# Performance work log

Measured on AMD Instinct MI355X. Metric: run time of the kernel, lower is better.

## Reference

```python
import jax, jax.numpy as jnp
import numpy as np
from jax import lax

L, S, H, D_IN, D_OUT = 4, 64, 256, 768, 768
B, T = 8, 2048
EPS = 1e-5


def _xavier(key, shape):
    fan_out, fan_in = shape[-2], shape[-1]
    limit = (6.0 / (fan_in + fan_out)) ** 0.5
    return jax.random.uniform(key, shape, jnp.float32, -limit, limit)


def setup_inputs() -> dict:
    key = jax.random.key(0)
    ks = jax.random.split(key, 12)
    return {
        "x": jax.random.normal(ks[0], (B, T, D_IN), jnp.float32),
        "in_proj_w": _xavier(ks[1], (H, D_IN)),
        "in_proj_b": jnp.zeros((H,), jnp.float32),
        "ln_g": jnp.ones((L, H), jnp.float32),
        "ln_b": jnp.zeros((L, H), jnp.float32),
        "ip_w": _xavier(ks[2], (L, S, H)),
        "ip_b": jnp.zeros((L, S), jnp.float32),
        "A": jax.random.normal(ks[3], (L, S, S), jnp.float32) * 0.1,
        "Bv": jax.random.normal(ks[4], (L, S), jnp.float32) * 0.1,
        "Cm": jax.random.normal(ks[5], (L, H, S), jnp.float32) * 0.1,
        "bias_A": jnp.zeros((L, S), jnp.float32),
        "bias_C": jnp.zeros((L, H), jnp.float32),
        "gate_w": _xavier(ks[6], (L, H, H)),
        "gate_b": jnp.zeros((L, H), jnp.float32),
        "proj_w": _xavier(ks[7], (L, H, H)),
        "proj_b": jnp.zeros((L, H), jnp.float32),
        "out_proj_w": _xavier(ks[8], (D_OUT, H)),
        "out_proj_b": jnp.zeros((D_OUT,), jnp.float32),
    }


def _layer_norm(x, g, b):
    mu = jnp.mean(x, axis=-1, keepdims=True)
    var = jnp.mean(jnp.square(x - mu), axis=-1, keepdims=True)
    return (x - mu) * lax.rsqrt(var + EPS) * g + b


def _ssm_layer(xn, ip_w, ip_b, A, Bv, Cm, bias_A, bias_C, gate_w, gate_b, proj_w, proj_b):
    # xn: [B, T, H]
    x_state = jnp.einsum("bth,sh->bts", xn, ip_w) + ip_b          # [B,T,S]
    gate = jax.nn.sigmoid(jnp.einsum("bth,gh->btg", xn, gate_w) + gate_b)  # [B,T,H]

    def step(h, xs_t):
        # h: [B,S], xs_t: [B,S]
        h = jnp.clip(h @ A.T + Bv * xs_t + bias_A, -10.0, 10.0)
        y = h @ Cm.T + bias_C                                     # [B,H]
        return h, y

    h0 = jnp.zeros((xn.shape[0], A.shape[0]), xn.dtype)
    _, ys = lax.scan(step, h0, jnp.swapaxes(x_state, 0, 1))        # ys: [T,B,H]
    y = jnp.swapaxes(ys, 0, 1)                                     # [B,T,H]
    y = jnp.einsum("bth,oh->bto", y, proj_w) + proj_b
    return gate * y + (1.0 - gate) * xn


def reference(x, in_proj_w, in_proj_b, ln_g, ln_b, ip_w, ip_b, A, Bv, Cm,
              bias_A, bias_C, gate_w, gate_b, proj_w, proj_b, out_proj_w, out_proj_b):
    h = jnp.einsum("btd,hd->bth", x, in_proj_w) + in_proj_b
    for i in range(L):
        xn = _layer_norm(h, ln_g[i], ln_b[i])
        h = h + _ssm_layer(xn, ip_w[i], ip_b[i], A[i], Bv[i], Cm[i],
                           bias_A[i], bias_C[i], gate_w[i], gate_b[i],
                           proj_w[i], proj_b[i])
    return jnp.einsum("bth,oh->bto", h, out_proj_w) + out_proj_b
```

## Files before the change

### kernel.cpp

```cpp
#include <hip/hip_runtime.h>

typedef float f32x4 __attribute__((ext_vector_type(4)));
typedef short short8 __attribute__((ext_vector_type(8)));

#define T_LEN 2048
#define HD 256
#define SD 64
#define DIN 768
#define DOUT 768
#define NCHUNK 32
#define CLEN 64

#define SBAR() __builtin_amdgcn_sched_barrier(0)

__device__ __forceinline__ unsigned short f2bf(float f) {
    unsigned int u = __float_as_uint(f);
    unsigned int r = u + 0x7FFFu + ((u >> 16) & 1u);
    return (unsigned short)(r >> 16);
}
__device__ __forceinline__ float bf2f(unsigned short h) {
    return __uint_as_float(((unsigned int)h) << 16);
}
__device__ __forceinline__ int swz(int row, int col, int stride) {
    return row * stride + (col ^ ((row & 7) << 3));
}
#define GLL(gp, lp) __builtin_amdgcn_global_load_lds( \
    (const __attribute__((address_space(1))) void*)(gp), \
    (__attribute__((address_space(3))) void*)(lp), 16, 0, 0)

__global__ __launch_bounds__(256) void cvt_w_k(const float* __restrict__ s0, const float* __restrict__ s1,
                                               const float* __restrict__ s2, const float* __restrict__ s3,
                                               const float* __restrict__ s4, const float* __restrict__ s5,
                                               unsigned short* __restrict__ d) {
    int i = blockIdx.x * 256 + threadIdx.x;
    if (i >= 1048576) return;
    float v;
    if (i < 196608)      v = s0[i];
    else if (i < 262144) v = s1[i - 196608];
    else if (i < 524288) v = s2[i - 262144];
    else if (i < 786432) v = s3[i - 524288];
    else if (i < 851968) v = s4[i - 786432];
    else                 v = s5[i - 851968];
    d[i] = f2bf(v);
}

__global__ __launch_bounds__(256) void matpow_k(const float* __restrict__ A, float* __restrict__ Apow) {
    __shared__ unsigned short Mh[4096], Ml[4096], MhT[4096], MlT[4096];
    const int l = blockIdx.x, tid = threadIdx.x;
    const int w = tid >> 6, ln = tid & 63, ll = ln & 15, lh = ln >> 4;
    const float* src = A + l * 4096;
    for (int i = tid; i < 4096; i += 256) {
        float v = src[i];
        unsigned short hi = f2bf(v);
        unsigned short lo = f2bf(v - bf2f(hi));
        int r = i >> 6, c = i & 63;
        Mh[swz(r, c, 64)] = hi;  Ml[swz(r, c, 64)] = lo;
        MhT[swz(c, r, 64)] = hi; MlT[swz(c, r, 64)] = lo;
    }
    __syncthreads();
    for (int it = 0; it < 6; it++) {
        f32x4 acc[4] = {};
#pragma unroll
        for (int ks = 0; ks < 2; ks++) {
            int ar = w * 16 + ll, c0 = ks * 32 + lh * 8;
            short8 ah = *reinterpret_cast<const short8*>(&Mh[swz(ar, c0, 64)]);
            short8 al = *reinterpret_cast<const short8*>(&Ml[swz(ar, c0, 64)]);
#pragma unroll
            for (int nf = 0; nf < 4; nf++) {
                int br = nf * 16 + ll;
                short8 bh = *reinterpret_cast<const short8*>(&MhT[swz(br, c0, 64)]);
                short8 bl = *reinterpret_cast<const short8*>(&MlT[swz(br, c0, 64)]);
                acc[nf] = __builtin_amdgcn_mfma_f32_16x16x32_bf16(ah, bh, acc[nf], 0, 0, 0);
                acc[nf] = __builtin_amdgcn_mfma_f32_16x16x32_bf16(ah, bl, acc[nf], 0, 0, 0);
                acc[nf] = __builtin_amdgcn_mfma_f32_16x16x32_bf16(al, bh, acc[nf], 0, 0, 0);
            }
        }
        __syncthreads();
#pragma unroll
        for (int nf = 0; nf < 4; nf++)
#pragma unroll
            for (int r = 0; r < 4; r++) {
                float v = acc[nf][r];
                int row = w * 16 + lh * 4 + r, col = nf * 16 + ll;
                unsigned short hi = f2bf(v);
                unsigned short lo = f2bf(v - bf2f(hi));
                Mh[swz(row, col, 64)] = hi;  Ml[swz(row, col, 64)] = lo;
                MhT[swz(col, row, 64)] = hi; MlT[swz(col, row, 64)] = lo;
            }
        __syncthreads();
    }
    for (int i = tid; i < 4096; i += 256) {
        int r = i >> 6, c = i & 63;
        Apow[l * 4096 + i] = bf2f(Mh[swz(r, c, 64)]) + bf2f(Ml[swz(r, c, 64)]);
    }
}

__global__ __launch_bounds__(256) void in_ln_k(const float* __restrict__ x,
                                               const unsigned short* __restrict__ w_in,
                                               const float* __restrict__ inb,
                                               const float* __restrict__ lng, const float* __restrict__ lnb,
                                               unsigned short* __restrict__ hb, unsigned short* __restrict__ xnb) {
    __shared__ unsigned short smem[8192 + 32 * 264];
    unsigned short* Ws = smem;
    unsigned short* hnb = smem + 8192;
    const int tid = threadIdx.x, l = tid & 63, w = tid >> 6;
    const int ll = l & 15, lh = l >> 4;
    const int mf = w >> 1, nh = w & 1;
    const int m0 = blockIdx.x * 32;
    const float* ap = x + (size_t)(m0 + mf * 16 + ll) * DIN + lh * 8;
    const unsigned short* gwb = w_in + (size_t)(w * 64 + (l >> 2)) * DIN + (l & 3) * 8;
    unsigned short* lwb = &Ws[(w * 64) * 32];
    f32x4 acc[8] = {};
    for (int k0 = 0; k0 < DIN; k0 += 32) {
#pragma unroll
        for (int q = 0; q < 4; q++)
            GLL(gwb + (size_t)(q * 16) * DIN + k0, lwb + q * 16 * 32);
        float4 a0 = *reinterpret_cast<const float4*>(ap + k0);
        float4 a1 = *reinterpret_cast<const float4*>(ap + k0 + 4);
        short8 af;
        af[0] = (short)f2bf(a0.x); af[1] = (short)f2bf(a0.y);
        af[2] = (short)f2bf(a0.z); af[3] = (short)f2bf(a0.w);
        af[4] = (short)f2bf(a1.x); af[5] = (short)f2bf(a1.y);
        af[6] = (short)f2bf(a1.z); af[7] = (short)f2bf(a1.w);
        __syncthreads();
#pragma unroll
        for (int j = 0; j < 8; j++) {
            short8 b = *reinterpret_cast<const short8*>(&Ws[(size_t)(nh * 128 + j * 16 + ll) * 32 + lh * 8]);
            acc[j] = __builtin_amdgcn_mfma_f32_16x16x32_bf16(af, b, acc[j], 0, 0, 0);
        }
        __syncthreads();
    }
#pragma unroll
    for (int j = 0; j < 8; j++)
#pragma unroll
        for (int r = 0; r < 4; r++) {
            int rowl = mf * 16 + lh * 4 + r;
            int col = nh * 128 + j * 16 + ll;
            hnb[rowl * 264 + col] = f2bf(acc[j][r] + inb[col]);
        }
    __syncthreads();
#pragma unroll
    for (int q = 0; q < 8; q++) {
        int rowl = w * 8 + q;
        size_t gidx = (size_t)(m0 + rowl) * HD + l * 4;
        ushort4 hv = *reinterpret_cast<const ushort4*>(&hnb[rowl * 264 + l * 4]);
        float o0 = bf2f(hv.x), o1 = bf2f(hv.y), o2 = bf2f(hv.z), o3 = bf2f(hv.w);
        float s = o0 + o1 + o2 + o3;
        float s2 = o0 * o0 + o1 * o1 + o2 * o2 + o3 * o3;
#pragma unroll
        for (int mm = 1; mm < 64; mm <<= 1) { s += __shfl_xor(s, mm); s2 += __shfl_xor(s2, mm); }
        float mean = s * (1.f / 256.f);
        float var = s2 * (1.f / 256.f) - mean * mean;
        float rstd = rsqrtf(var + 1e-5f);
        int c = l * 4;
        *reinterpret_cast<ushort4*>(hb + gidx) = hv;
        ushort4 xo;
        xo.x = f2bf((o0 - mean) * rstd * lng[c + 0] + lnb[c + 0]);
        xo.y = f2bf((o1 - mean) * rstd * lng[c + 1] + lnb[c + 1]);
        xo.z = f2bf((o2 - mean) * rstd * lng[c + 2] + lnb[c + 2]);
        xo.w = f2bf((o3 - mean) * rstd * lng[c + 3] + lnb[c + 3]);
        *reinterpret_cast<ushort4*>(xnb + gidx) = xo;
    }
}

__device__ __forceinline__ void staged_core256(const unsigned short* __restrict__ A, int m0b,
                                               const unsigned short* __restrict__ W, int n0,
                                               unsigned short* As, unsigned short* Bs,
                                               int tid, f32x4 (*acc)[4]) {
    const int l = tid & 63, w = tid >> 6;
    const int ll = l & 15, lh = l >> 4;
    const int lr = l >> 2, lc = (l & 3) * 8;
    const unsigned short* ga1 = A + (size_t)(m0b + w * 32 + lr) * 256 + lc;
    const unsigned short* ga2 = ga1 + 16 * 256;
    const unsigned short* gb  = W + (size_t)(n0 + w * 16 + lr) * 256 + lc;
    unsigned short* la1 = As + w * 1024;
    unsigned short* la2 = As + w * 1024 + 512;
    unsigned short* lb  = Bs + w * 512;
#pragma unroll
    for (int k0 = 0; k0 < 256; k0 += 32) {
        GLL(ga1 + k0, la1);
        GLL(ga2 + k0, la2);
        GLL(gb + k0, lb);
        __syncthreads();
        short8 a0 = *reinterpret_cast<const short8*>(&As[(w * 32 + ll) * 32 + lh * 8]);
        short8 a1 = *reinterpret_cast<const short8*>(&As[(w * 32 + 16 + ll) * 32 + lh * 8]);
        short8 b0 = *reinterpret_cast<const short8*>(&Bs[(ll) * 32 + lh * 8]);
        short8 b1 = *reinterpret_cast<const short8*>(&Bs[(16 + ll) * 32 + lh * 8]);
        short8 b2 = *reinterpret_cast<const short8*>(&Bs[(32 + ll) * 32 + lh * 8]);
        short8 b3 = *reinterpret_cast<const short8*>(&Bs[(48 + ll) * 32 + lh * 8]);
        acc[0][0] = __builtin_amdgcn_mfma_f32_16x16x32_bf16(a0, b0, acc[0][0], 0, 0, 0);
        acc[0][1] = __builtin_amdgcn_mfma_f32_16x16x32_bf16(a0, b1, acc[0][1], 0, 0, 0);
        acc[0][2] = __builtin_amdgcn_mfma_f32_16x16x32_bf16(a0, b2, acc[0][2], 0, 0, 0);
        acc[0][3] = __builtin_amdgcn_mfma_f32_16x16x32_bf16(a0, b3, acc[0][3], 0, 0, 0);
        acc[1][0] = __builtin_amdgcn_mfma_f32_16x16x32_bf16(a1, b0, acc[1][0], 0, 0, 0);
        acc[1][1] = __builtin_amdgcn_mfma_f32_16x16x32_bf16(a1, b1, acc[1][1], 0, 0, 0);
        acc[1][2] = __builtin_amdgcn_mfma_f32_16x16x32_bf16(a1, b2, acc[1][2], 0, 0, 0);
        acc[1][3] = __builtin_amdgcn_mfma_f32_16x16x32_bf16(a1, b3, acc[1][3], 0, 0, 0);
        __syncthreads();
    }
}

template <int N>
__global__ __launch_bounds__(256) void gemm_k(const unsigned short* __restrict__ A,
                                              const unsigned short* __restrict__ W,
                                              const float* __restrict__ bias,
                                              float* __restrict__ outf) {
    __shared__ char smem[128 * 68 * 4];
    unsigned short* As = (unsigned short*)smem;
    unsigned short* Bs = As + 4096;
    float* sf = (float*)smem;
    const int tid = threadIdx.x, l = tid & 63, w = tid >> 6;
    const int ll = l & 15, lh = l >> 4;
    const int m0b = blockIdx.x * 128;
    const int n0 = blockIdx.y * 64;
    f32x4 acc[2][4] = {};
    staged_core256(A, m0b, W, n0, As, Bs, tid, acc);
#pragma unroll
    for (int mf = 0; mf < 2; mf++)
#pragma unroll
        for (int nf = 0; nf < 4; nf++)
#pragma unroll
            for (int r = 0; r < 4; r++) {
                int rowl = w * 32 + mf * 16 + lh * 4 + r;
                int col = nf * 16 + ll;
                sf[rowl * 68 + col] = acc[mf][nf][r] + bias[n0 + col];
            }
    __syncthreads();
#pragma unroll
    for (int p = 0; p < 8; p++) {
        int rowl = p * 16 + (tid >> 4);
        int col = (tid & 15) * 4;
        f32x4 v = *reinterpret_cast<const f32x4*>(&sf[rowl * 68 + col]);
        __builtin_nontemporal_store(v, reinterpret_cast<f32x4*>(outf + (size_t)(m0b + rowl) * N + n0 + col));
    }
}

__global__ __launch_bounds__(256) void gateip_k(const unsigned short* __restrict__ xnb,
                                                const unsigned short* __restrict__ wg,
                                                const unsigned short* __restrict__ wip,
                                                const float* __restrict__ gbias, const float* __restrict__ ipb,
                                                const float* __restrict__ Bv, const float* __restrict__ bA,
                                                unsigned short* __restrict__ gB, float* __restrict__ u) {
    __shared__ char smem[128 * 68 * 4];
    unsigned short* As = (unsigned short*)smem;
    unsigned short* Bs = As + 4096;
    float* sf = (float*)smem;
    unsigned short* su = (unsigned short*)smem;
    const int tid = threadIdx.x, l = tid & 63, w = tid >> 6;
    const int ll = l & 15, lh = l >> 4;
    const int m0b = blockIdx.x * 128;
    const int y = blockIdx.y;
    const bool gate = (y < 4);
    const int n0 = gate ? y * 64 : 0;
    f32x4 acc[2][4] = {};
    staged_core256(xnb, m0b, gate ? wg : wip, n0, As, Bs, tid, acc);
    if (gate) {
#pragma unroll
        for (int mf = 0; mf < 2; mf++)
#pragma unroll
            for (int nf = 0; nf < 4; nf++)
#pragma unroll
                for (int r = 0; r < 4; r++) {
                    int rowl = w * 32 + mf * 16 + lh * 4 + r;
                    int col = nf * 16 + ll;
                    float v = acc[mf][nf][r] + gbias[n0 + col];
                    su[rowl * 72 + col] = f2bf(1.f / (1.f + __expf(-v)));
                }
        __syncthreads();
#pragma unroll
        for (int p = 0; p < 8; p++) {
            int rowl = p * 16 + (tid >> 4);
            int col = (tid & 15) * 4;
            ushort4 v = *reinterpret_cast<const ushort4*>(&su[rowl * 72 + col]);
            *reinterpret_cast<ushort4*>(gB + (size_t)(m0b + rowl) * HD + n0 + col) = v;
        }
    } else {
#pragma unroll
        for (int mf = 0; mf < 2; mf++)
#pragma unroll
            for (int nf = 0; nf < 4; nf++)
#pragma unroll
                for (int r = 0; r < 4; r++) {
                    int rowl = w * 32 + mf * 16 + lh * 4 + r;
                    int col = nf * 16 + ll;
                    float v = acc[mf][nf][r] + ipb[col];
                    sf[rowl * 68 + col] = Bv[col] * v + bA[col];
                }
        __syncthreads();
#pragma unroll
        for (int p = 0; p < 8; p++) {
            int rowl = p * 16 + (tid >> 4);
            int col = (tid & 15) * 4;
            int m = m0b + rowl;
            int t = m & 2047, b2 = m >> 11;
            float4 v = *reinterpret_cast<const float4*>(&sf[rowl * 68 + col]);
            *reinterpret_cast<float4*>(u + ((size_t)((t << 3) + b2)) * 64 + col) = v;
        }
    }
}

template <bool LAST>
__global__ __launch_bounds__(256) void post3_k(const unsigned short* __restrict__ Hs,
                                               const unsigned short* __restrict__ wc,
                                               const float* __restrict__ bC,
                                               const unsigned short* __restrict__ wp,
                                               const float* __restrict__ pb,
                                               const unsigned short* __restrict__ gB,
                                               unsigned short* __restrict__ xnb,
                                               unsigned short* __restrict__ hb,
                                               const float* __restrict__ lng2, const float* __restrict__ lnb2) {
    __shared__ unsigned short ys[32 * 256];
    __shared__ unsigned short hnb[32 * 264];
    const int tid = threadIdx.x, l = tid & 63, w = tid >> 6;
    const int ll = l & 15, lh = l >> 4;
    const int mf = w >> 1, nh = w & 1;
    const int m0 = blockIdx.x * 32;
    {
        short8 ha[2], cb[8][2];
        const unsigned short* Ap = Hs + (size_t)(m0 + mf * 16 + ll) * SD + lh * 8;
#pragma unroll
        for (int ks = 0; ks < 2; ks++)
            ha[ks] = *reinterpret_cast<const short8*>(Ap + ks * 32);
#pragma unroll
        for (int ks = 0; ks < 2; ks++)
#pragma unroll
            for (int j = 0; j < 8; j++)
                cb[j][ks] = *reinterpret_cast<const short8*>(wc + (size_t)((nh * 8 + j) * 16 + ll) * SD + ks * 32 + lh * 8);
        SBAR();
        f32x4 acc[8] = {};
#pragma unroll
        for (int ks = 0; ks < 2; ks++)
#pragma unroll
            for (int j = 0; j < 8; j++)
                acc[j] = __builtin_amdgcn_mfma_f32_16x16x32_bf16(ha[ks], cb[j][ks], acc[j], 0, 0, 0);
#pragma unroll
        for (int j = 0; j < 8; j++)
#pragma unroll
            for (int r = 0; r < 4; r++) {
                int rowl = mf * 16 + lh * 4 + r;
                int col = (nh * 8 + j) * 16 + ll;
                ys[swz(rowl, col, 256)] = f2bf(acc[j][r] + bC[col]);
            }
    }
    __syncthreads();
    {
        f32x4 acc2[8] = {};
        const int arow = mf * 16 + ll;
#pragma unroll
        for (int kb = 0; kb < 4; kb++) {
            short8 pwf[8][2];
#pragma unroll
            for (int ks = 0; ks < 2; ks++)
#pragma unroll
                for (int j = 0; j < 8; j++)
                    pwf[j][ks] = *reinterpret_cast<const short8*>(wp + (size_t)((nh * 8 + j) * 16 + ll) * HD + kb * 64 + ks * 32 + lh * 8);
            SBAR();
#pragma unroll
            for (int ks = 0; ks < 2; ks++) {
                int c0 = kb * 64 + ks * 32 + lh * 8;
                short8 a = *reinterpret_cast<const short8*>(&ys[swz(arow, c0, 256)]);
#pragma unroll
                for (int j = 0; j < 8; j++)
                    acc2[j] = __builtin_amdgcn_mfma_f32_16x16x32_bf16(a, pwf[j][ks], acc2[j], 0, 0, 0);
            }
        }
#pragma unroll
        for (int j = 0; j < 8; j++)
#pragma unroll
            for (int r = 0; r < 4; r++) {
                int rowl = mf * 16 + lh * 4 + r;
                int col = (nh * 8 + j) * 16 + ll;
                hnb[rowl * 264 + col] = f2bf(acc2[j][r] + pb[col]);
            }
    }
    __syncthreads();
#pragma unroll
    for (int q = 0; q < 8; q++) {
        int rowl = w * 8 + q;
        int m = m0 + rowl;
        int t = m >> 3, b2 = m & 7;
        size_t gidx = ((size_t)((b2 << 11) + t)) * HD + l * 4;
        ushort4 hv = *reinterpret_cast<const ushort4*>(hb + gidx);
        ushort4 gv = *reinterpret_cast<const ushort4*>(gB + gidx);
        ushort4 xv = *reinterpret_cast<const ushort4*>(xnb + gidx);
        ushort4 yv = *reinterpret_cast<const ushort4*>(&hnb[rowl * 264 + l * 4]);
        float g0 = bf2f(gv.x), g1 = bf2f(gv.y), g2 = bf2f(gv.z), g3 = bf2f(gv.w);
        float o0 = bf2f(hv.x) + g0 * bf2f(yv.x) + (1.f - g0) * bf2f(xv.x);
        float o1 = bf2f(hv.y) + g1 * bf2f(yv.y) + (1.f - g1) * bf2f(xv.y);
        float o2 = bf2f(hv.z) + g2 * bf2f(yv.z) + (1.f - g2) * bf2f(xv.z);
        float o3 = bf2f(hv.w) + g3 * bf2f(yv.w) + (1.f - g3) * bf2f(xv.w);
        ushort4 hbv;
        hbv.x = f2bf(o0); hbv.y = f2bf(o1); hbv.z = f2bf(o2); hbv.w = f2bf(o3);
        *reinterpret_cast<ushort4*>(hb + gidx) = hbv;
        if constexpr (!LAST) {
            float s = o0 + o1 + o2 + o3;
            float s2 = o0 * o0 + o1 * o1 + o2 * o2 + o3 * o3;
#pragma unroll
            for (int mm = 1; mm < 64; mm <<= 1) { s += __shfl_xor(s, mm); s2 += __shfl_xor(s2, mm); }
            float mean = s * (1.f / 256.f);
            float var = s2 * (1.f / 256.f) - mean * mean;
            float rstd = rsqrtf(var + 1e-5f);
            int c = l * 4;
            ushort4 xo;
            xo.x = f2bf((o0 - mean) * rstd * lng2[c + 0] + lnb2[c + 0]);
            xo.y = f2bf((o1 - mean) * rstd * lng2[c + 1] + lnb2[c + 1]);
            xo.z = f2bf((o2 - mean) * rstd * lng2[c + 2] + lnb2[c + 2]);
            xo.w = f2bf((o3 - mean) * rstd * lng2[c + 3] + lnb2[c + 3]);
            *reinterpret_cast<ushort4*>(xnb + gidx) = xo;
        }
    }
}

__device__ __forceinline__ void loadA64(const float* __restrict__ Af, int s, float* a) {
#pragma unroll
    for (int q = 0; q < 16; q++) {
        float4 v = reinterpret_cast<const float4*>(Af + s * 64)[q];
        a[q * 4 + 0] = v.x; a[q * 4 + 1] = v.y; a[q * 4 + 2] = v.z; a[q * 4 + 3] = v.w;
    }
}

__device__ __forceinline__ float step64(const float* a, float h, float uu) {
    float ac0 = uu, ac1 = 0.f, ac2 = 0.f, ac3 = 0.f;
#pragma unroll
    for (int k = 0; k < 64; k += 4) {
        float b0 = __int_as_float(__builtin_amdgcn_readlane(__float_as_int(h), k + 0));
        float b1 = __int_as_float(__builtin_amdgcn_readlane(__float_as_int(h), k + 1));
        float b2 = __int_as_float(__builtin_amdgcn_readlane(__float_as_int(h), k + 2));
        float b3 = __int_as_float(__builtin_amdgcn_readlane(__float_as_int(h), k + 3));
        ac0 = fmaf(b0, a[k + 0], ac0);
        ac1 = fmaf(b1, a[k + 1], ac1);
        ac2 = fmaf(b2, a[k + 2], ac2);
        ac3 = fmaf(b3, a[k + 3], ac3);
    }
    return (ac0 + ac1) + (ac2 + ac3);
}

__global__ __launch_bounds__(64) void scan_chunk_k(const float* __restrict__ Af,
                                                   const float* __restrict__ u,
                                                   float* __restrict__ Slast) {
    const int c = blockIdx.x >> 3, b = blockIdx.x & 7;
    const int s = threadIdx.x;
    float a[64];
    loadA64(Af, s, a);
    const float* up = u + (c * CLEN) * 512 + b * 64 + s;
    float uv[CLEN];
#pragma unroll
    for (int i = 0; i < CLEN; i++) uv[i] = up[i * 512];
    float h = 0.f;
#pragma unroll
    for (int i = 0; i < CLEN; i++) h = step64(a, h, uv[i]);
    Slast[blockIdx.x * 64 + s] = h;
}

__global__ __launch_bounds__(64) void replay_k(const float* __restrict__ Af,
                                               const float* __restrict__ Apow,
                                               const float* __restrict__ u,
                                               const float* __restrict__ Slast,
                                               unsigned short* __restrict__ Hs,
                                               int* __restrict__ flag) {
    const int c = blockIdx.x >> 3, b = blockIdx.x & 7;
    const int s = threadIdx.x;
    float a[64];
    float carry = 0.f;
    if (c > 0) {
        loadA64(Apow, s, a);
        for (int j = 0; j < c; j++) {
            float sl = Slast[(j * 8 + b) * 64 + s];
            carry = step64(a, carry, sl);
        }
    }
    loadA64(Af, s, a);
    const float* up = u + (c * CLEN) * 512 + b * 64 + s;
    float uv[CLEN];
#pragma unroll
    for (int i = 0; i < CLEN; i++) uv[i] = up[i * 512];
    float h = carry;
    unsigned short* hp = Hs + (c * CLEN) * 512 + b * 64 + s;
    bool bad = false;
#pragma unroll
    for (int i = 0; i < CLEN; i++) {
        h = step64(a, h, uv[i]);
        bad |= (fabsf(h) > 10.f);
        hp[i * 512] = f2bf(h);
    }
    if (__any(bad ? 1 : 0)) {
        if (s == 0) atomicOr(flag, 1);
    }
}

__global__ __launch_bounds__(64) void scan_seq_k(const float* __restrict__ Af,
                                                 const float* __restrict__ u,
                                                 unsigned short* __restrict__ Hs,
                                                 const int* __restrict__ flag) {
    if (*flag == 0) return;
    const int b = blockIdx.x;
    const int s = threadIdx.x;
    float a[64];
    loadA64(Af, s, a);
    float h = 0.f;
    for (int t = 0; t < T_LEN; t++) {
        float uu = u[((t << 3) + b) * 64 + s];
        float hp = step64(a, h, uu);
        h = fminf(fmaxf(hp, -10.f), 10.f);
        Hs[((t << 3) + b) * 64 + s] = f2bf(h);
    }
}

extern "C" void kernel_launch(void* const* d_in, const int* in_sizes, int n_in,
                              void* d_out, int out_size, void* d_ws, size_t ws_size,
                              hipStream_t stream) {
    const float* x    = (const float*)d_in[0];
    const float* inw  = (const float*)d_in[1];
    const float* inb  = (const float*)d_in[2];
    const float* lng  = (const float*)d_in[3];
    const float* lnb  = (const float*)d_in[4];
    const float* ipw  = (const float*)d_in[5];
    const float* ipb  = (const float*)d_in[6];
    const float* Amat = (const float*)d_in[7];
    const float* Bv   = (const float*)d_in[8];
    const float* Cm   = (const float*)d_in[9];
    const float* bA   = (const float*)d_in[10];
    const float* bC   = (const float*)d_in[11];
    const float* gw   = (const float*)d_in[12];
    const float* gbia = (const float*)d_in[13];
    const float* pw   = (const float*)d_in[14];
    const float* pb   = (const float*)d_in[15];
    const float* ow   = (const float*)d_in[16];
    const float* ob   = (const float*)d_in[17];

    char* ws = (char*)d_ws;
    float*          u  = (float*)(ws + 0);
    unsigned short* Hs = (unsigned short*)(ws + 4194304);
    unsigned short* hb = (unsigned short*)(ws + 14680064);
    unsigned short* wb = (unsigned short*)(ws + 25165824);
    unsigned short* xnb = (unsigned short*)(ws + 44040192);
    unsigned short* gB  = (unsigned short*)(ws + 52428800);

    char* sc = (char*)d_out;
    float* Apow  = (float*)(sc + 0);
    float* Slast = (float*)(sc + 65536);
    int*   flag  = (int*)(sc + 196608);

    const unsigned short* w_in = wb + 0;
    const unsigned short* w_ip = wb + 196608;
    const unsigned short* w_g  = wb + 262144;
    const unsigned short* w_p  = wb + 524288;
    const unsigned short* w_c  = wb + 786432;
    const unsigned short* w_o  = wb + 851968;

    hipMemsetAsync(flag, 0, 16, stream);
    cvt_w_k<<<4096, 256, 0, stream>>>(inw, ipw, gw, pw, Cm, ow, wb);
    matpow_k<<<4, 256, 0, stream>>>(Amat, Apow);

    in_ln_k<<<512, 256, 0, stream>>>(x, w_in, inb, lng, lnb, hb, xnb);
    for (int i = 0; i < 4; i++) {
        gateip_k<<<dim3(128, 5), 256, 0, stream>>>(xnb, w_g + i * 65536, w_ip + i * 16384,
                                                   gbia + i * HD, ipb + i * SD,
                                                   Bv + i * SD, bA + i * SD, gB, u);
        scan_chunk_k<<<256, 64, 0, stream>>>(Amat + i * 4096, u, Slast);
        replay_k<<<256, 64, 0, stream>>>(Amat + i * 4096, Apow + i * 4096, u, Slast, Hs, flag + i);
        scan_seq_k<<<8, 64, 0, stream>>>(Amat + i * 4096, u, Hs, flag + i);
        if (i < 3)
            post3_k<false><<<512, 256, 0, stream>>>(Hs, w_c + i * 16384, bC + i * HD,
                                                    w_p + i * 65536, pb + i * HD, gB, xnb, hb,
                                                    lng + (i + 1) * HD, lnb + (i + 1) * HD);
        else
            post3_k<true><<<512, 256, 0, stream>>>(Hs, w_c + i * 16384, bC + i * HD,
                                                   w_p + i * 65536, pb + i * HD, gB, xnb, hb,
                                                   lng, lnb);
    }
    gemm_k<DOUT><<<dim3(128, 12), 256, 0, stream>>>(hb, w_o, ob, (float*)d_out);
}
```

Before: 408.0 us.

## Double K-tile depth to 64 with XOR-swizzled LDS layout in GEMM cores

The input-projection kernel and the shared 256-wide GEMM core now stage 64-wide K slices per iteration instead of 32, halving the number of barrier pairs and load rounds. LDS tiles are written with an XOR swizzle on 8-element column groups and read back with the matching swizzle, to avoid bank conflicts on the wider 128-byte rows. Shared-memory usage for the in_ln kernel grows, and Bs offsets in the GEMM kernels move to fit the larger A tile. Higher LDS footprint could lower occupancy.

```diff
diff --git a/kernel.cpp b/kernel.cpp
--- a/kernel.cpp
+++ b/kernel.cpp
@@ -100,33 +100,44 @@
                                                const float* __restrict__ inb,
                                                const float* __restrict__ lng, const float* __restrict__ lnb,
                                                unsigned short* __restrict__ hb, unsigned short* __restrict__ xnb) {
-    __shared__ unsigned short smem[8192 + 32 * 264];
+    __shared__ unsigned short smem[16384 + 32 * 264];
     unsigned short* Ws = smem;
-    unsigned short* hnb = smem + 8192;
+    unsigned short* hnb = smem + 16384;
     const int tid = threadIdx.x, l = tid & 63, w = tid >> 6;
     const int ll = l & 15, lh = l >> 4;
     const int mf = w >> 1, nh = w & 1;
     const int m0 = blockIdx.x * 32;
+    const int r8 = l >> 3;
+    const int csw = ((l & 7) ^ r8) * 8;
     const float* ap = x + (size_t)(m0 + mf * 16 + ll) * DIN + lh * 8;
-    const unsigned short* gwb = w_in + (size_t)(w * 64 + (l >> 2)) * DIN + (l & 3) * 8;
-    unsigned short* lwb = &Ws[(w * 64) * 32];
+    const unsigned short* gwR = w_in + (size_t)(w * 8 + r8) * DIN + csw;
+    unsigned short* lwR = Ws + (size_t)(w * 8) * 64 + l * 8;
     f32x4 acc[8] = {};
-    for (int k0 = 0; k0 < DIN; k0 += 32) {
-#pragma unroll
-        for (int q = 0; q < 4; q++)
-            GLL(gwb + (size_t)(q * 16) * DIN + k0, lwb + q * 16 * 32);
-        float4 a0 = *reinterpret_cast<const float4*>(ap + k0);
-        float4 a1 = *reinterpret_cast<const float4*>(ap + k0 + 4);
-        short8 af;
-        af[0] = (short)f2bf(a0.x); af[1] = (short)f2bf(a0.y);
-        af[2] = (short)f2bf(a0.z); af[3] = (short)f2bf(a0.w);
-        af[4] = (short)f2bf(a1.x); af[5] = (short)f2bf(a1.y);
-        af[6] = (short)f2bf(a1.z); af[7] = (short)f2bf(a1.w);
-        __syncthreads();
-#pragma unroll
-        for (int j = 0; j < 8; j++) {
-            short8 b = *reinterpret_cast<const short8*>(&Ws[(size_t)(nh * 128 + j * 16 + ll) * 32 + lh * 8]);
-            acc[j] = __builtin_amdgcn_mfma_f32_16x16x32_bf16(af, b, acc[j], 0, 0, 0);
+    for (int k0 = 0; k0 < DIN; k0 += 64) {
+#pragma unroll
+        for (int q = 0; q < 8; q++)
+            GLL(gwR + (size_t)(q * 32) * DIN + k0, lwR + q * 32 * 64);
+        short8 af[2];
+#pragma unroll
+        for (int ks = 0; ks < 2; ks++) {
+            float4 a0 = *reinterpret_cast<const float4*>(ap + k0 + ks * 32);
+            float4 a1 = *reinterpret_cast<const float4*>(ap + k0 + ks * 32 + 4);
+            short8 t;
+            t[0] = (short)f2bf(a0.x); t[1] = (short)f2bf(a0.y);
+            t[2] = (short)f2bf(a0.z); t[3] = (short)f2bf(a0.w);
+            t[4] = (short)f2bf(a1.x); t[5] = (short)f2bf(a1.y);
+            t[6] = (short)f2bf(a1.z); t[7] = (short)f2bf(a1.w);
+            af[ks] = t;
+        }
+        __syncthreads();
+#pragma unroll
+        for (int ks = 0; ks < 2; ks++) {
+            const int so = (((ks * 4 + lh) ^ (ll & 7)) * 8);
+#pragma unroll
+            for (int j = 0; j < 8; j++) {
+                short8 b = *reinterpret_cast<const short8*>(&Ws[(size_t)(nh * 128 + j * 16 + ll) * 64 + so]);
+                acc[j] = __builtin_amdgcn_mfma_f32_16x16x32_bf16(af[ks], b, acc[j], 0, 0, 0);
+            }
         }
         __syncthreads();
     }
@@ -169,33 +180,39 @@
                                                int tid, f32x4 (*acc)[4]) {
     const int l = tid & 63, w = tid >> 6;
     const int ll = l & 15, lh = l >> 4;
-    const int lr = l >> 2, lc = (l & 3) * 8;
-    const unsigned short* ga1 = A + (size_t)(m0b + w * 32 + lr) * 256 + lc;
-    const unsigned short* ga2 = ga1 + 16 * 256;
-    const unsigned short* gb  = W + (size_t)(n0 + w * 16 + lr) * 256 + lc;
-    unsigned short* la1 = As + w * 1024;
-    unsigned short* la2 = As + w * 1024 + 512;
-    unsigned short* lb  = Bs + w * 512;
-#pragma unroll
-    for (int k0 = 0; k0 < 256; k0 += 32) {
-        GLL(ga1 + k0, la1);
-        GLL(ga2 + k0, la2);
-        GLL(gb + k0, lb);
-        __syncthreads();
-        short8 a0 = *reinterpret_cast<const short8*>(&As[(w * 32 + ll) * 32 + lh * 8]);
-        short8 a1 = *reinterpret_cast<const short8*>(&As[(w * 32 + 16 + ll) * 32 + lh * 8]);
-        short8 b0 = *reinterpret_cast<const short8*>(&Bs[(ll) * 32 + lh * 8]);
-        short8 b1 = *reinterpret_cast<const short8*>(&Bs[(16 + ll) * 32 + lh * 8]);
-        short8 b2 = *reinterpret_cast<const short8*>(&Bs[(32 + ll) * 32 + lh * 8]);
-        short8 b3 = *reinterpret_cast<const short8*>(&Bs[(48 + ll) * 32 + lh * 8]);
-        acc[0][0] = __builtin_amdgcn_mfma_f32_16x16x32_bf16(a0, b0, acc[0][0], 0, 0, 0);
-        acc[0][1] = __builtin_amdgcn_mfma_f32_16x16x32_bf16(a0, b1, acc[0][1], 0, 0, 0);
-        acc[0][2] = __builtin_amdgcn_mfma_f32_16x16x32_bf16(a0, b2, acc[0][2], 0, 0, 0);
-        acc[0][3] = __builtin_amdgcn_mfma_f32_16x16x32_bf16(a0, b3, acc[0][3], 0, 0, 0);
-        acc[1][0] = __builtin_amdgcn_mfma_f32_16x16x32_bf16(a1, b0, acc[1][0], 0, 0, 0);
-        acc[1][1] = __builtin_amdgcn_mfma_f32_16x16x32_bf16(a1, b1, acc[1][1], 0, 0, 0);
-        acc[1][2] = __builtin_amdgcn_mfma_f32_16x16x32_bf16(a1, b2, acc[1][2], 0, 0, 0);
-        acc[1][3] = __builtin_amdgcn_mfma_f32_16x16x32_bf16(a1, b3, acc[1][3], 0, 0, 0);
+    const int r8 = l >> 3;
+    const int csw = ((l & 7) ^ r8) * 8;
+    const unsigned short* gaR = A + (size_t)(m0b + w * 8 + r8) * 256 + csw;
+    const unsigned short* gbR = W + (size_t)(n0 + w * 8 + r8) * 256 + csw;
+    unsigned short* laR = As + (size_t)(w * 8) * 64 + l * 8;
+    unsigned short* lbR = Bs + (size_t)(w * 8) * 64 + l * 8;
+#pragma unroll
+    for (int k0 = 0; k0 < 256; k0 += 64) {
+#pragma unroll
+        for (int q = 0; q < 4; q++)
+            GLL(gaR + (size_t)(q * 32) * 256 + k0, laR + q * 32 * 64);
+#pragma unroll
+        for (int q = 0; q < 2; q++)
+            GLL(gbR + (size_t)(q * 32) * 256 + k0, lbR + q * 32 * 64);
+        __syncthreads();
+#pragma unroll
+        for (int ks = 0; ks < 2; ks++) {
+            const int so = (((ks * 4 + lh) ^ (ll & 7)) * 8);
+            short8 a0 = *reinterpret_cast<const short8*>(&As[(size_t)(w * 32 + ll) * 64 + so]);
+            short8 a1 = *reinterpret_cast<const short8*>(&As[(size_t)(w * 32 + 16 + ll) * 64 + so]);
+            short8 b0 = *reinterpret_cast<const short8*>(&Bs[(size_t)(ll) * 64 + so]);
+            short8 b1 = *reinterpret_cast<const short8*>(&Bs[(size_t)(16 + ll) * 64 + so]);
+            short8 b2 = *reinterpret_cast<const short8*>(&Bs[(size_t)(32 + ll) * 64 + so]);
+            short8 b3 = *reinterpret_cast<const short8*>(&Bs[(size_t)(48 + ll) * 64 + so]);
+            acc[0][0] = __builtin_amdgcn_mfma_f32_16x16x32_bf16(a0, b0, acc[0][0], 0, 0, 0);
+            acc[0][1] = __builtin_amdgcn_mfma_f32_16x16x32_bf16(a0, b1, acc[0][1], 0, 0, 0);
+            acc[0][2] = __builtin_amdgcn_mfma_f32_16x16x32_bf16(a0, b2, acc[0][2], 0, 0, 0);
+            acc[0][3] = __builtin_amdgcn_mfma_f32_16x16x32_bf16(a0, b3, acc[0][3], 0, 0, 0);
+            acc[1][0] = __builtin_amdgcn_mfma_f32_16x16x32_bf16(a1, b0, acc[1][0], 0, 0, 0);
+            acc[1][1] = __builtin_amdgcn_mfma_f32_16x16x32_bf16(a1, b1, acc[1][1], 0, 0, 0);
+            acc[1][2] = __builtin_amdgcn_mfma_f32_16x16x32_bf16(a1, b2, acc[1][2], 0, 0, 0);
+            acc[1][3] = __builtin_amdgcn_mfma_f32_16x16x32_bf16(a1, b3, acc[1][3], 0, 0, 0);
+        }
         __syncthreads();
     }
 }
@@ -207,7 +224,7 @@
                                               float* __restrict__ outf) {
     __shared__ char smem[128 * 68 * 4];
     unsigned short* As = (unsigned short*)smem;
-    unsigned short* Bs = As + 4096;
+    unsigned short* Bs = As + 8192;
     float* sf = (float*)smem;
     const int tid = threadIdx.x, l = tid & 63, w = tid >> 6;
     const int ll = l & 15, lh = l >> 4;
@@ -243,7 +260,7 @@
                                                 unsigned short* __restrict__ gB, float* __restrict__ u) {
     __shared__ char smem[128 * 68 * 4];
     unsigned short* As = (unsigned short*)smem;
-    unsigned short* Bs = As + 4096;
+    unsigned short* Bs = As + 8192;
     float* sf = (float*)smem;
     unsigned short* su = (unsigned short*)smem;
     const int tid = threadIdx.x, l = tid & 63, w = tid >> 6;
```

After: 407.6 us. Within noise of the previous version (-0.1%).
